# Kernel optimization log

Hardware: AMD Instinct MI355X
Metric: run time of the kernel (lower is better)

The kernel has to match this reference:

```python
import jax, jax.numpy as jnp
import numpy as np

BUCKET_SIZE = 64
N_HASHES = 8
SELF_ATTN_MASK_VAL = -10000.0


def look_one_back(x):
    # concat each chunk with the previous chunk along the within-chunk axis (axis=2)
    prev = jnp.concatenate([x[:, -1:], x[:, :-1]], axis=1)
    return jnp.concatenate([x, prev], axis=2)


def setup_inputs() -> dict:
    key = jax.random.key(0)
    b, s, d = 4, 4096, 64
    n_buckets = s // BUCKET_SIZE  # 64
    kq, kk, kv, kr = jax.random.split(key, 4)
    return {
        "q": jax.random.normal(kq, (b, s, d), jnp.float32),
        "k": jax.random.normal(kk, (b, s, d), jnp.float32),
        "v": jax.random.normal(kv, (b, s, d), jnp.float32),
        "rotations": jax.random.normal(kr, (d, N_HASHES, n_buckets // 2), jnp.float32),
    }


def reference(q, k, v, rotations):
    b, s, d = q.shape
    n_buckets = s // BUCKET_SIZE
    n_chunks = N_HASHES * n_buckets

    # ---- hash_vectors: random-rotation LSH bucketing on q ----
    rot = jnp.einsum('bsd,dhn->bhsn', q, rotations)           # [b, nh, s, nb/2]
    rot = jnp.concatenate([rot, -rot], axis=-1)               # [b, nh, s, nb]
    buckets = jnp.argmax(rot, axis=-1)                        # [b, nh, s]
    offsets = (jnp.arange(N_HASHES) * n_buckets)[None, :, None]
    buckets = (buckets + offsets).reshape(b, N_HASHES * s)    # [b, nh*s]

    # ---- sort tokens by (bucket, position) ----
    ticker = jnp.broadcast_to(jnp.arange(N_HASHES * s), (b, N_HASHES * s))
    buckets_and_t = s * buckets + (ticker % s)
    sticker = jnp.argsort(buckets_and_t, axis=-1)             # sort permutation
    sbuckets_and_t = jnp.take_along_axis(buckets_and_t, sticker, axis=-1)
    undo_sort = jnp.argsort(sticker, axis=-1)
    st = sticker % s                                          # original positions

    gather_seq = lambda x, idx: jnp.take_along_axis(x, idx[..., None], axis=1)
    sq = gather_seq(q, st)
    sk = gather_seq(k, st)
    sv = gather_seq(v, st)

    bq_t = st.reshape(b, n_chunks, -1)                        # [b, n, s_c]
    bq = sq.reshape(b, n_chunks, -1, d)
    bk = sk.reshape(b, n_chunks, -1, d)
    bv = sv.reshape(b, n_chunks, -1, d)

    bk = bk / jnp.linalg.norm(bk, axis=-1, keepdims=True)
    bk = look_one_back(bk)                                    # [b, n, 2*s_c, d]
    bv = look_one_back(bv)
    bkv_t = look_one_back(bq_t)                               # [b, n, 2*s_c]

    dots = jnp.einsum('bnsd,bnzd->bnsz', bq, bk) * (d ** -0.5)
    masked_value = -jnp.finfo(dots.dtype).max

    # self-attention mask (soft, matches torch SELF_ATTN_MASK_VAL)
    self_mask = bq_t[:, :, :, None] == bkv_t[:, :, None, :]
    dots = jnp.where(self_mask, SELF_ATTN_MASK_VAL, dots)

    # do not attend across buckets
    bq_buckets = (sbuckets_and_t // s).reshape(b, n_chunks, -1)
    bkv_buckets = look_one_back(bq_buckets)
    bucket_mask = bq_buckets[:, :, :, None] != bkv_buckets[:, :, None, :]
    dots = jnp.where(bucket_mask, masked_value, dots)

    # duplicate-attention correction
    locs1 = undo_sort // BUCKET_SIZE
    locs2 = (locs1 + 1) % n_chunks
    locs1 = buckets * n_chunks + locs1
    locs2 = buckets * n_chunks + locs2
    locs = jnp.concatenate([locs1.reshape(b, N_HASHES, s),
                            locs2.reshape(b, N_HASHES, s)], axis=1)
    locs = jnp.transpose(locs, (0, 2, 1))                     # [b, s, 2*nh]
    slocs = jnp.take_along_axis(locs, st[..., None], axis=1)  # [b, nh*s, 2*nh]
    b_locs = slocs.reshape(b, n_chunks, -1, 2 * N_HASHES)
    bq_locs = jnp.concatenate([b_locs[..., :N_HASHES], b_locs[..., :N_HASHES]], axis=-1)
    bkv_locs = look_one_back(b_locs)                          # [b, n, 2*s_c, 2*nh]
    dup_counts = jnp.sum(bq_locs[:, :, :, None, :] == bkv_locs[:, :, None, :, :], axis=-1)
    dots = dots - jnp.log(dup_counts.astype(dots.dtype) + 1e-9)

    # softmax (stable) and attention output
    dots_lse = jax.nn.logsumexp(dots, axis=-1, keepdims=True)
    probs_chunk = jnp.exp(dots - dots_lse)
    bo = jnp.einsum('bnsz,bnzd->bnsd', probs_chunk, bv)

    # unsort and combine across hash rounds
    so = bo.reshape(b, -1, d)
    o = jnp.take_along_axis(so, undo_sort[..., None], axis=1).reshape(b, N_HASHES, s, d)
    slogits = dots_lse.reshape(b, -1)
    logits = jnp.take_along_axis(slogits, undo_sort, axis=1).reshape(b, N_HASHES, s, 1)
    probs = jnp.exp(logits - jax.nn.logsumexp(logits, axis=1, keepdims=True))
    out = jnp.sum(o * probs, axis=1)                          # [b, s, d]
    return out
```

## Files before the change

kernel.cpp:

```cpp
#include <hip/hip_runtime.h>
#include <hip/hip_bf16.h>
#include <math.h>

constexpr int B   = 4;
constexpr int S   = 4096;
constexpr int D   = 64;
constexpr int NH  = 8;
constexpr int NB  = 64;
constexpr int NBT = 512;
constexpr int NI  = NH * S;
constexpr int NCH = 512;
constexpr int CHB = 256;

typedef __attribute__((ext_vector_type(8))) _Float16 f16x8;
typedef __attribute__((ext_vector_type(2))) __fp16 fp16x2;
typedef __attribute__((ext_vector_type(4))) float f32x4;
typedef __attribute__((ext_vector_type(2))) unsigned short u16x2;

__device__ __forceinline__ unsigned short f16b(float x) {
    _Float16 h = (_Float16)x;
    return __builtin_bit_cast(unsigned short, h);
}
__device__ __forceinline__ u16x2 nm2(int a, int b) {
    u16x2 x = __builtin_bit_cast(u16x2, a ^ b);
    u16x2 one = {1, 1};
    return __builtin_elementwise_min(x, one);
}
__device__ __forceinline__ unsigned pk16(float a, float b) {
    fp16x2 hp = __builtin_amdgcn_cvt_pkrtz(a, b);
    return __builtin_bit_cast(unsigned, hp);
}
template <int CTRL>
__device__ __forceinline__ float dppf(float x) {
    return __builtin_bit_cast(float,
        __builtin_amdgcn_update_dpp(__builtin_bit_cast(int, x), __builtin_bit_cast(int, x),
                                    CTRL, 0xF, 0xF, false));
}

__global__ void k_prep(const float* __restrict__ q, const float* __restrict__ k,
                       const float* __restrict__ v, unsigned short* __restrict__ q16,
                       unsigned short* __restrict__ kn16, unsigned short* __restrict__ v16) {
    int row  = blockIdx.x * 4 + (threadIdx.x >> 6);
    int lane = threadIdx.x & 63;
    size_t idx = (size_t)row * 64 + lane;
    float kv = k[idx];
    float ss = kv * kv;
#pragma unroll
    for (int m = 1; m < 64; m <<= 1) ss += __shfl_xor(ss, m, 64);
    kn16[idx] = f16b(kv / sqrtf(ss));
    q16[idx]  = f16b(q[idx] * 0.125f);
    v16[idx]  = f16b(v[idx]);
}

__global__ __launch_bounds__(256)
void k_hash(const float* __restrict__ q, const float* __restrict__ rot,
            int* __restrict__ buckets, int* __restrict__ counts) {
    int blk = blockIdx.x;
    int tko = blk & 31, h = (blk >> 5) & 7, b = blk >> 8;
    __shared__ __align__(16) float rs[64 * 36];
    __shared__ int hist[64];
    if (threadIdx.x < 64) hist[threadIdx.x] = 0;
    for (int i = threadIdx.x; i < 2048; i += 256) {
        int nn = i & 31, d = i >> 5;
        rs[d * 36 + nn] = rot[(d * 8 + h) * 32 + nn];
    }
    __syncthreads();
    int tid = threadIdx.x;
    int ng = tid & 7, tg = tid >> 3;
    int t0 = tko * 128 + tg * 4;
    const float* qp = q + ((size_t)b * S + t0) * 64;
    float acc[4][4] = {};
    #pragma unroll 4
    for (int d4 = 0; d4 < 16; ++d4) {
        f32x4 r4[4];
        #pragma unroll
        for (int dd = 0; dd < 4; ++dd)
            r4[dd] = *(const f32x4*)(rs + (4 * d4 + dd) * 36 + 4 * ng);
        #pragma unroll
        for (int i = 0; i < 4; ++i) {
            f32x4 q4 = *(const f32x4*)(qp + i * 64 + d4 * 4);
            #pragma unroll
            for (int dd = 0; dd < 4; ++dd)
                #pragma unroll
                for (int c = 0; c < 4; ++c)
                    acc[i][c] += q4[dd] * r4[dd][c];
        }
    }
    #pragma unroll
    for (int i = 0; i < 4; ++i) {
        float vp = -3.402823466e38f, vn = -3.402823466e38f;
        int ip = 0, in_ = 0;
        #pragma unroll
        for (int c = 0; c < 4; ++c) {
            float a = acc[i][c]; int idx = 4 * ng + c;
            if (a > vp)  { vp = a;  ip = idx; }
            if (-a > vn) { vn = -a; in_ = idx; }
        }
        #pragma unroll
        for (int off = 1; off < 8; off <<= 1) {
            float ov = __shfl_xor(vp, off); int oi = __shfl_xor(ip, off);
            if (ov > vp || (ov == vp && oi < ip)) { vp = ov; ip = oi; }
            ov = __shfl_xor(vn, off); oi = __shfl_xor(in_, off);
            if (ov > vn || (ov == vn && oi < in_)) { vn = ov; in_ = oi; }
        }
        if (ng == 0) {
            int bi = (vn > vp) ? (in_ + 32) : ip;
            buckets[b * NI + h * 4096 + t0 + i] = bi + h * NB;
            atomicAdd(&hist[bi], 1);
        }
    }
    __syncthreads();
    int cglob = h * 32 + tko;
    int* cw = counts + ((size_t)b * CHB + cglob) * NBT;
    for (int j = tid; j < NBT; j += 256) {
        int local = j - h * 64;
        cw[j] = (local >= 0 && local < 64) ? hist[local] : 0;
    }
}

__global__ void k_scan1(int* __restrict__ counts, int* __restrict__ tot) {
    int bkt = blockIdx.x & 511, b = blockIdx.x >> 9;
    int lane = threadIdx.x;
    size_t i0 = ((size_t)b * CHB + 4 * lane) * NBT + bkt;
    int v0 = counts[i0], v1 = counts[i0 + NBT], v2 = counts[i0 + 2 * NBT], v3 = counts[i0 + 3 * NBT];
    int s = v0 + v1 + v2 + v3;
    int incl = s;
    #pragma unroll
    for (int off = 1; off < 64; off <<= 1) {
        int t = __shfl_up(incl, off);
        if (lane >= off) incl += t;
    }
    int excl = incl - s;
    counts[i0]           = excl;
    counts[i0 + NBT]     = excl + v0;
    counts[i0 + 2 * NBT] = excl + v0 + v1;
    counts[i0 + 3 * NBT] = excl + v0 + v1 + v2;
    if (lane == 63) tot[b * NBT + bkt] = incl;
}

__global__ void k_scatter(const int* __restrict__ buckets, const int* __restrict__ counts,
                          const int* __restrict__ tot, int* __restrict__ spos,
                          int* __restrict__ undo) {
    int b = blockIdx.x >> 8, c = blockIdx.x & 255;
    __shared__ int bk_s[128];
    __shared__ int sbase[NBT];
    __shared__ int wsum[2];
    int tid = threadIdx.x;
    int4 tv = *(const int4*)(tot + b * NBT + tid * 4);
    int part = tv.x + tv.y + tv.z + tv.w;
    int incl = part;
    int lane = tid & 63, w = tid >> 6;
    #pragma unroll
    for (int off = 1; off < 64; off <<= 1) {
        int t = __shfl_up(incl, off);
        if (lane >= off) incl += t;
    }
    if (lane == 63) wsum[w] = incl;
    int i_flat = c * 128 + tid;
    int bkt = buckets[b * NI + i_flat];
    bk_s[tid] = bkt;
    __syncthreads();
    if (w == 1) incl += wsum[0];
    int excl = incl - part;
    sbase[4 * tid]     = excl;
    sbase[4 * tid + 1] = excl + tv.x;
    sbase[4 * tid + 2] = excl + tv.x + tv.y;
    sbase[4 * tid + 3] = excl + tv.x + tv.y + tv.z;
    __syncthreads();
    int rank = 0;
    for (int j = 0; j < 128; ++j) {
        int vv = bk_s[j];
        rank += (j < tid && vv == bkt);
    }
    int pos = sbase[bkt] + counts[((size_t)b * CHB + c) * NBT + bkt] + rank;
    spos[b * NI + pos] = (i_flat & 4095) | (bkt << 12);
    undo[b * NI + i_flat] = pos;
}

__global__ void k_locP(const int* __restrict__ buckets, const int* __restrict__ undo,
                       int4* __restrict__ loc1P) {
    int idx = blockIdx.x * 256 + threadIdx.x;
    int b = idx >> 12, t = idx & 4095;
    int v1[8];
    #pragma unroll
    for (int h = 0; h < 8; ++h) {
        int i = b * NI + (h << 12) + t;
        int lo = (buckets[i] & 63) << 9;
        int ch = undo[i] >> 6;
        v1[h] = lo | ch;
    }
    loc1P[idx] = make_int4(v1[0] | (v1[1] << 16), v1[2] | (v1[3] << 16),
                           v1[4] | (v1[5] << 16), v1[6] | (v1[7] << 16));
}

__device__ __forceinline__ int bump_loc(int k1) {
    return (k1 & 0x7E007E00) | ((k1 + 0x00010001) & 0x01FF01FF);
}

__global__ __launch_bounds__(256, 2)
void k_attn(const unsigned short* __restrict__ q16, const unsigned short* __restrict__ kn16,
            const unsigned short* __restrict__ v16, const int* __restrict__ spos,
            const int4* __restrict__ loc1P, unsigned short* __restrict__ soh,
            float* __restrict__ slog) {
    int n = blockIdx.x & 511, b = blockIdx.x >> 9;
    __shared__ __align__(16) char buf[31488];
    unsigned short* qs = (unsigned short*)buf;
    unsigned short* ks = (unsigned short*)(buf + 9216);
    unsigned short* ph = (unsigned short*)buf;
    unsigned short* vh = (unsigned short*)(buf + 9216);
    int* klocs1 = (int*)(buf + 27648);
    int* qlocs  = (int*)(buf + 29696);
    int* mq     = (int*)(buf + 30720);
    int* mk     = (int*)(buf + 30976);

    int tid = threadIdx.x;
    int bni = b * NI;
    const unsigned short* q16b = q16 + ((size_t)b << 12) * 64;
    const unsigned short* kn16b = kn16 + ((size_t)b << 12) * 64;
    const unsigned short* v16b = v16 + ((size_t)b << 12) * 64;

    if (tid < 64) mq[tid] = spos[bni + n * 64 + tid];
    else if (tid < 192) {
        int z = tid - 64;
        int nn = (z < 64) ? n : ((n + 511) & 511);
        mk[z] = spos[bni + nn * 64 + (z & 63)];
    }
    __syncthreads();

    #pragma unroll
    for (int it = 0; it < 2; ++it) {
        int i = it * 256 + tid;
        int row = i >> 3, c8 = i & 7;
        int t = mq[row] & 4095;
        uint4 val = *(const uint4*)(q16b + (size_t)t * 64 + c8 * 8);
        *(uint4*)(qs + row * 72 + c8 * 8) = val;
    }
    #pragma unroll
    for (int it = 0; it < 4; ++it) {
        int i = it * 256 + tid;
        int row = i >> 3, c8 = i & 7;
        int t = mk[row] & 4095;
        uint4 val = *(const uint4*)(kn16b + (size_t)t * 64 + c8 * 8);
        *(uint4*)(ks + row * 72 + c8 * 8) = val;
    }
    if (tid < 128) {
        int t = mk[tid] & 4095;
        *(int4*)(klocs1 + tid * 4) = loc1P[((size_t)b << 12) | t];
    } else if (tid < 192) {
        int r = tid - 128;
        int tq = mq[r] & 4095;
        *(int4*)(qlocs + r * 4) = loc1P[((size_t)b << 12) | tq];
    }
    __syncthreads();

    int li = tid & 15, hi4 = (tid >> 4) & 3, w = tid >> 6;

    f32x4 sacc[8];
    {
        f16x8 a0 = *(f16x8*)(qs + (16 * w + li) * 72 + 8 * hi4);
        f16x8 a1 = *(f16x8*)(qs + (16 * w + li) * 72 + 32 + 8 * hi4);
        #pragma unroll
        for (int zt = 0; zt < 8; ++zt) {
            f16x8 b0 = *(f16x8*)(ks + (16 * zt + li) * 72 + 8 * hi4);
            f16x8 b1 = *(f16x8*)(ks + (16 * zt + li) * 72 + 32 + 8 * hi4);
            f32x4 c = {0.f, 0.f, 0.f, 0.f};
            c = __builtin_amdgcn_mfma_f32_16x16x32_f16(a0, b0, c, 0, 0, 0);
            c = __builtin_amdgcn_mfma_f32_16x16x32_f16(a1, b1, c, 0, 0, 0);
            sacc[zt] = c;
        }
    }

    int tqr[4], bqr[4];
    int4 lq[4];
    #pragma unroll
    for (int j = 0; j < 4; ++j) {
        int R = 16 * w + 4 * hi4 + j;
        int m = mq[R];
        tqr[j] = m & 4095; bqr[j] = m >> 12;
        lq[j] = *(const int4*)(qlocs + R * 4);
    }
    #pragma unroll
    for (int zt = 0; zt < 8; ++zt) {
        int z = 16 * zt + li;
        int mz = mk[z]; int tk = mz & 4095, bk = mz >> 12;
        int4 k1 = *(const int4*)(klocs1 + z * 4);
        int4 k2;
        k2.x = bump_loc(k1.x); k2.y = bump_loc(k1.y);
        k2.z = bump_loc(k1.z); k2.w = bump_loc(k1.w);
        #pragma unroll
        for (int j = 0; j < 4; ++j) {
            float s = sacc[zt][j];
            if (tqr[j] == tk) s = -10000.0f;
            if (bqr[j] != bk) s = -3.402823466e38f;
            u16x2 acc = nm2(lq[j].x, k1.x);
            acc = acc + nm2(lq[j].y, k1.y);
            acc = acc + nm2(lq[j].z, k1.z);
            acc = acc + nm2(lq[j].w, k1.w);
            acc = acc + nm2(lq[j].x, k2.x);
            acc = acc + nm2(lq[j].y, k2.y);
            acc = acc + nm2(lq[j].z, k2.z);
            acc = acc + nm2(lq[j].w, k2.w);
            unsigned ua = __builtin_bit_cast(unsigned, acc);
            int dup = 16 - (int)((ua & 0xffffu) + (ua >> 16));
            s -= __logf(fmaxf((float)dup, 1.0f));
            sacc[zt][j] = s;
        }
    }

    float inv[4];
    #pragma unroll
    for (int j = 0; j < 4; ++j) {
        float m = sacc[0][j];
        #pragma unroll
        for (int zt = 1; zt < 8; ++zt) m = fmaxf(m, sacc[zt][j]);
        m = fmaxf(m, dppf<0x121>(m));
        m = fmaxf(m, dppf<0x122>(m));
        m = fmaxf(m, dppf<0x124>(m));
        m = fmaxf(m, dppf<0x128>(m));
        float sum = 0.f;
        #pragma unroll
        for (int zt = 0; zt < 8; ++zt) {
            float e = __expf(sacc[zt][j] - m);
            sacc[zt][j] = e; sum += e;
        }
        sum += dppf<0x121>(sum);
        sum += dppf<0x122>(sum);
        sum += dppf<0x124>(sum);
        sum += dppf<0x128>(sum);
        float lse = m + __logf(sum);
        inv[j] = 1.0f / sum;
        if (li == 0) slog[bni + n * 64 + 16 * w + 4 * hi4 + j] = lse;
    }
    __syncthreads();

    #pragma unroll
    for (int it = 0; it < 8; ++it) {
        int i = it * 256 + tid;
        int zp = i & 63;
        int dp = i >> 6;
        int t0 = mk[2 * zp] & 4095, t1 = mk[2 * zp + 1] & 4095;
        unsigned a = *(const unsigned*)(v16b + (size_t)t0 * 64 + 2 * dp);
        unsigned c = *(const unsigned*)(v16b + (size_t)t1 * 64 + 2 * dp);
        *(unsigned*)(vh + (2 * dp) * 136 + 2 * zp)     = __builtin_amdgcn_perm(c, a, 0x05040100u);
        *(unsigned*)(vh + (2 * dp + 1) * 136 + 2 * zp) = __builtin_amdgcn_perm(c, a, 0x07060302u);
    }
    f32x4 oacc[4] = {{0,0,0,0},{0,0,0,0},{0,0,0,0},{0,0,0,0}};
    #pragma unroll
    for (int half = 0; half < 2; ++half) {
        #pragma unroll
        for (int zt4 = 0; zt4 < 4; ++zt4) {
            int zt = half * 4 + zt4;
            #pragma unroll
            for (int j = 0; j < 4; ++j) {
                float p  = sacc[zt][j] * inv[j];
                float po = dppf<0xB1>(p);
                if ((li & 1) == 0) {
                    int R  = 16 * w + 4 * hi4 + j;
                    int zl = 16 * zt4 + li;
                    *(unsigned*)(ph + R * 72 + zl) = pk16(p, po);
                }
            }
        }
        __syncthreads();
        #pragma unroll
        for (int step = 0; step < 2; ++step) {
            f16x8 pa = *(f16x8*)(ph + (16 * w + li) * 72 + 32 * step + 8 * hi4);
            #pragma unroll
            for (int nt = 0; nt < 4; ++nt) {
                f16x8 vb = *(f16x8*)(vh + (16 * nt + li) * 136 + 64 * half + 32 * step + 8 * hi4);
                oacc[nt] = __builtin_amdgcn_mfma_f32_16x16x32_f16(pa, vb, oacc[nt], 0, 0, 0);
            }
        }
        __syncthreads();
    }

    size_t ob = ((size_t)bni + n * 64) * 64;
    #pragma unroll
    for (int nt = 0; nt < 4; ++nt)
        #pragma unroll
        for (int j = 0; j < 4; ++j) {
            float o  = oacc[nt][j];
            float oo = dppf<0xB1>(o);
            if ((li & 1) == 0) {
                *(unsigned*)(soh + ob + (size_t)(16 * w + 4 * hi4 + j) * 64 + 16 * nt + li) =
                    pk16(o, oo);
            }
        }
}

__global__ void k_comb(const int* __restrict__ undo, const float* __restrict__ slog,
                       const unsigned short* __restrict__ soh, float* __restrict__ out) {
    int flatT = blockIdx.x * 4 + (threadIdx.x >> 6);
    int lane  = threadIdx.x & 63;
    int b = flatT >> 12, t = flatT & (S - 1);
    int ph[NH]; float lg[NH];
    float m = -3.402823466e38f;
#pragma unroll
    for (int h = 0; h < NH; ++h) {
        ph[h] = undo[b * NI + (h << 12) + t];
        lg[h] = slog[b * NI + ph[h]];
        m = fmaxf(m, lg[h]);
    }
    float sum = 0.f;
#pragma unroll
    for (int h = 0; h < NH; ++h) sum += __expf(lg[h] - m);
    float lse2 = m + __logf(sum);
    float o = 0.f;
#pragma unroll
    for (int h = 0; h < NH; ++h) {
        float wgt = __expf(lg[h] - lse2);
        _Float16 hv = *(const _Float16*)(soh + ((size_t)b * NI + ph[h]) * D + lane);
        o += wgt * (float)hv;
    }
    out[(size_t)flatT * D + lane] = o;
}

extern "C" void kernel_launch(void* const* d_in, const int* in_sizes, int n_in,
                              void* d_out, int out_size, void* d_ws, size_t ws_size,
                              hipStream_t stream) {
    const float* q   = (const float*)d_in[0];
    const float* k   = (const float*)d_in[1];
    const float* v   = (const float*)d_in[2];
    const float* rot = (const float*)d_in[3];
    float* out = (float*)d_out;

    char* ws = (char*)d_ws;
    size_t off = 0;
    auto alloc = [&](size_t bytes) -> void* {
        void* p = ws + off;
        off += (bytes + 255) & ~(size_t)255;
        return p;
    };
    unsigned short* q16  = (unsigned short*)alloc((size_t)B * S * D * 2);
    unsigned short* kn16 = (unsigned short*)alloc((size_t)B * S * D * 2);
    unsigned short* v16  = (unsigned short*)alloc((size_t)B * S * D * 2);
    unsigned short* soh  = (unsigned short*)alloc((size_t)B * NI * D * 2);
    float* slog    = (float*)alloc((size_t)B * NI * 4);
    int*   buckets = (int*)alloc((size_t)B * NI * 4);
    int*   counts  = (int*)alloc((size_t)B * CHB * NBT * 4);
    int*   tot     = (int*)alloc((size_t)B * NBT * 4);
    int*   spos    = (int*)alloc((size_t)B * NI * 4);
    int*   undo    = (int*)alloc((size_t)B * NI * 4);
    int4*  loc1P   = (int4*)alloc((size_t)B * S * 16);

    k_prep<<<B * S / 4, 256, 0, stream>>>(q, k, v, q16, kn16, v16);
    k_hash<<<1024, 256, 0, stream>>>(q, rot, buckets, counts);
    k_scan1<<<B * NBT, 64, 0, stream>>>(counts, tot);
    k_scatter<<<B * CHB, 128, 0, stream>>>(buckets, counts, tot, spos, undo);
    k_locP<<<B * S / 256, 256, 0, stream>>>(buckets, undo, loc1P);
    k_attn<<<B * NCH, 256, 0, stream>>>(q16, kn16, v16, spos, loc1P, soh, slog);
    k_comb<<<B * S / 4, 256, 0, stream>>>(undo, slog, soh, out);
}
```

Before: 106.4 us.

## Fuse prep, scan and loc kernels into hash/scatter and switch softmax to base-2

```diff
diff --git a/kernel.cpp b/kernel.cpp
--- a/kernel.cpp
+++ b/kernel.cpp
@@ -17,9 +17,14 @@
 typedef __attribute__((ext_vector_type(4))) float f32x4;
 typedef __attribute__((ext_vector_type(2))) unsigned short u16x2;
 
+constexpr float LOG2E = 1.44269504088896341f;
+
 __device__ __forceinline__ unsigned short f16b(float x) {
     _Float16 h = (_Float16)x;
     return __builtin_bit_cast(unsigned short, h);
+}
+__device__ __forceinline__ unsigned pk_rne(float a, float b) {
+    return (unsigned)f16b(a) | ((unsigned)f16b(b) << 16);
 }
 __device__ __forceinline__ u16x2 nm2(int a, int b) {
     u16x2 x = __builtin_bit_cast(u16x2, a ^ b);
@@ -37,35 +42,23 @@
                                     CTRL, 0xF, 0xF, false));
 }
 
-__global__ void k_prep(const float* __restrict__ q, const float* __restrict__ k,
-                       const float* __restrict__ v, unsigned short* __restrict__ q16,
-                       unsigned short* __restrict__ kn16, unsigned short* __restrict__ v16) {
-    int row  = blockIdx.x * 4 + (threadIdx.x >> 6);
-    int lane = threadIdx.x & 63;
-    size_t idx = (size_t)row * 64 + lane;
-    float kv = k[idx];
-    float ss = kv * kv;
-#pragma unroll
-    for (int m = 1; m < 64; m <<= 1) ss += __shfl_xor(ss, m, 64);
-    kn16[idx] = f16b(kv / sqrtf(ss));
-    q16[idx]  = f16b(q[idx] * 0.125f);
-    v16[idx]  = f16b(v[idx]);
-}
-
 __global__ __launch_bounds__(256)
-void k_hash(const float* __restrict__ q, const float* __restrict__ rot,
-            int* __restrict__ buckets, int* __restrict__ counts) {
+void k_hash(const float* __restrict__ q, const float* __restrict__ k,
+            const float* __restrict__ v, const float* __restrict__ rot,
+            int* __restrict__ buckets, int* __restrict__ counts, int* __restrict__ tot,
+            unsigned short* __restrict__ q16, unsigned short* __restrict__ kn16,
+            unsigned short* __restrict__ v16) {
     int blk = blockIdx.x;
     int tko = blk & 31, h = (blk >> 5) & 7, b = blk >> 8;
     __shared__ __align__(16) float rs[64 * 36];
     __shared__ int hist[64];
-    if (threadIdx.x < 64) hist[threadIdx.x] = 0;
-    for (int i = threadIdx.x; i < 2048; i += 256) {
+    int tid = threadIdx.x;
+    if (tid < 64) hist[tid] = 0;
+    for (int i = tid; i < 2048; i += 256) {
         int nn = i & 31, d = i >> 5;
         rs[d * 36 + nn] = rot[(d * 8 + h) * 32 + nn];
     }
     __syncthreads();
-    int tid = threadIdx.x;
     int ng = tid & 7, tg = tid >> 3;
     int t0 = tko * 128 + tg * 4;
     const float* qp = q + ((size_t)b * S + t0) * 64;
@@ -110,55 +103,95 @@
         }
     }
     __syncthreads();
-    int cglob = h * 32 + tko;
-    int* cw = counts + ((size_t)b * CHB + cglob) * NBT;
-    for (int j = tid; j < NBT; j += 256) {
-        int local = j - h * 64;
-        cw[j] = (local >= 0 && local < 64) ? hist[local] : 0;
-    }
-}
-
-__global__ void k_scan1(int* __restrict__ counts, int* __restrict__ tot) {
-    int bkt = blockIdx.x & 511, b = blockIdx.x >> 9;
-    int lane = threadIdx.x;
-    size_t i0 = ((size_t)b * CHB + 4 * lane) * NBT + bkt;
-    int v0 = counts[i0], v1 = counts[i0 + NBT], v2 = counts[i0 + 2 * NBT], v3 = counts[i0 + 3 * NBT];
-    int s = v0 + v1 + v2 + v3;
-    int incl = s;
-    #pragma unroll
-    for (int off = 1; off < 64; off <<= 1) {
-        int t = __shfl_up(incl, off);
-        if (lane >= off) incl += t;
-    }
-    int excl = incl - s;
-    counts[i0]           = excl;
-    counts[i0 + NBT]     = excl + v0;
-    counts[i0 + 2 * NBT] = excl + v0 + v1;
-    counts[i0 + 3 * NBT] = excl + v0 + v1 + v2;
-    if (lane == 63) tot[b * NBT + bkt] = incl;
+    if (tid < 64) {
+        int cnt = hist[tid];
+        counts[((size_t)b * NBT + h * 64 + tid) * 32 + tko] = cnt;
+        atomicAdd(&tot[b * NBT + h * 64 + tid], cnt);
+    }
+
+    if (h == 0) {
+        int r  = tko * 128 + (tid >> 1);
+        int hf = tid & 1;
+        size_t base = ((size_t)b * S + r) * 64 + hf * 32;
+        f32x4 rv[8];
+        float ss = 0.f;
+        #pragma unroll
+        for (int j = 0; j < 8; ++j) {
+            rv[j] = *(const f32x4*)(k + base + 4 * j);
+            ss += rv[j][0]*rv[j][0] + rv[j][1]*rv[j][1] + rv[j][2]*rv[j][2] + rv[j][3]*rv[j][3];
+        }
+        ss += __shfl_xor(ss, 1);
+        float sc = rsqrtf(ss);
+        unsigned ow[16];
+        #pragma unroll
+        for (int i = 0; i < 16; ++i) {
+            float a  = rv[i >> 1][(i & 1) * 2] * sc;
+            float bb = rv[i >> 1][(i & 1) * 2 + 1] * sc;
+            ow[i] = pk_rne(a, bb);
+        }
+        *(uint4*)(kn16 + base)      = make_uint4(ow[0], ow[1], ow[2], ow[3]);
+        *(uint4*)(kn16 + base + 8)  = make_uint4(ow[4], ow[5], ow[6], ow[7]);
+        *(uint4*)(kn16 + base + 16) = make_uint4(ow[8], ow[9], ow[10], ow[11]);
+        *(uint4*)(kn16 + base + 24) = make_uint4(ow[12], ow[13], ow[14], ow[15]);
+        const float qsc = 0.125f * LOG2E;
+        #pragma unroll
+        for (int j = 0; j < 8; ++j) rv[j] = *(const f32x4*)(q + base + 4 * j);
+        #pragma unroll
+        for (int i = 0; i < 16; ++i)
+            ow[i] = pk_rne(rv[i >> 1][(i & 1) * 2] * qsc, rv[i >> 1][(i & 1) * 2 + 1] * qsc);
+        *(uint4*)(q16 + base)      = make_uint4(ow[0], ow[1], ow[2], ow[3]);
+        *(uint4*)(q16 + base + 8)  = make_uint4(ow[4], ow[5], ow[6], ow[7]);
+        *(uint4*)(q16 + base + 16) = make_uint4(ow[8], ow[9], ow[10], ow[11]);
+        *(uint4*)(q16 + base + 24) = make_uint4(ow[12], ow[13], ow[14], ow[15]);
+        #pragma unroll
+        for (int j = 0; j < 8; ++j) rv[j] = *(const f32x4*)(v + base + 4 * j);
+        #pragma unroll
+        for (int i = 0; i < 16; ++i)
+            ow[i] = pk_rne(rv[i >> 1][(i & 1) * 2], rv[i >> 1][(i & 1) * 2 + 1]);
+        *(uint4*)(v16 + base)      = make_uint4(ow[0], ow[1], ow[2], ow[3]);
+        *(uint4*)(v16 + base + 8)  = make_uint4(ow[4], ow[5], ow[6], ow[7]);
+        *(uint4*)(v16 + base + 16) = make_uint4(ow[8], ow[9], ow[10], ow[11]);
+        *(uint4*)(v16 + base + 24) = make_uint4(ow[12], ow[13], ow[14], ow[15]);
+    }
 }
 
 __global__ void k_scatter(const int* __restrict__ buckets, const int* __restrict__ counts,
                           const int* __restrict__ tot, int* __restrict__ spos,
-                          int* __restrict__ undo) {
+                          int* __restrict__ undo, unsigned short* __restrict__ locU) {
     int b = blockIdx.x >> 8, c = blockIdx.x & 255;
+    int h = c >> 5, tko = c & 31;
     __shared__ int bk_s[128];
     __shared__ int sbase[NBT];
+    __shared__ int pfx[64];
     __shared__ int wsum[2];
     int tid = threadIdx.x;
+    int lane = tid & 63, w = tid >> 6;
     int4 tv = *(const int4*)(tot + b * NBT + tid * 4);
     int part = tv.x + tv.y + tv.z + tv.w;
     int incl = part;
-    int lane = tid & 63, w = tid >> 6;
     #pragma unroll
     for (int off = 1; off < 64; off <<= 1) {
-        int t = __shfl_up(incl, off);
-        if (lane >= off) incl += t;
+        int t_ = __shfl_up(incl, off);
+        if (lane >= off) incl += t_;
     }
     if (lane == 63) wsum[w] = incl;
+    int bl = tid >> 1, hf = tid & 1;
+    const int* crow = counts + ((size_t)b * NBT + h * 64 + bl) * 32 + hf * 16;
+    int ps = 0;
+    #pragma unroll
+    for (int jj = 0; jj < 4; ++jj) {
+        int4 cv = *(const int4*)(crow + jj * 4);
+        int bi = hf * 16 + jj * 4;
+        ps += (bi + 0 < tko) ? cv.x : 0;
+        ps += (bi + 1 < tko) ? cv.y : 0;
+        ps += (bi + 2 < tko) ? cv.z : 0;
+        ps += (bi + 3 < tko) ? cv.w : 0;
+    }
+    ps += __shfl_xor(ps, 1);
     int i_flat = c * 128 + tid;
     int bkt = buckets[b * NI + i_flat];
     bk_s[tid] = bkt;
+    if (hf == 0) pfx[bl] = ps;
     __syncthreads();
     if (w == 1) incl += wsum[0];
     int excl = incl - part;
@@ -172,25 +205,12 @@
         int vv = bk_s[j];
         rank += (j < tid && vv == bkt);
     }
-    int pos = sbase[bkt] + counts[((size_t)b * CHB + c) * NBT + bkt] + rank;
+    int pos = sbase[bkt] + pfx[bkt - h * 64] + rank;
     spos[b * NI + pos] = (i_flat & 4095) | (bkt << 12);
     undo[b * NI + i_flat] = pos;
-}
-
-__global__ void k_locP(const int* __restrict__ buckets, const int* __restrict__ undo,
-                       int4* __restrict__ loc1P) {
-    int idx = blockIdx.x * 256 + threadIdx.x;
-    int b = idx >> 12, t = idx & 4095;
-    int v1[8];
-    #pragma unroll
-    for (int h = 0; h < 8; ++h) {
-        int i = b * NI + (h << 12) + t;
-        int lo = (buckets[i] & 63) << 9;
-        int ch = undo[i] >> 6;
-        v1[h] = lo | ch;
-    }
-    loc1P[idx] = make_int4(v1[0] | (v1[1] << 16), v1[2] | (v1[3] << 16),
-                           v1[4] | (v1[5] << 16), v1[6] | (v1[7] << 16));
+    int t = i_flat & 4095;
+    locU[(((size_t)b << 12) | t) * 8 + h] =
+        (unsigned short)(((bkt & 63) << 9) | (pos >> 6));
 }
 
 __device__ __forceinline__ int bump_loc(int k1) {
@@ -290,7 +310,7 @@
         #pragma unroll
         for (int j = 0; j < 4; ++j) {
             float s = sacc[zt][j];
-            if (tqr[j] == tk) s = -10000.0f;
+            if (tqr[j] == tk) s = -14426.950408f;
             if (bqr[j] != bk) s = -3.402823466e38f;
             u16x2 acc = nm2(lq[j].x, k1.x);
             acc = acc + nm2(lq[j].y, k1.y);
@@ -302,7 +322,7 @@
             acc = acc + nm2(lq[j].w, k2.w);
             unsigned ua = __builtin_bit_cast(unsigned, acc);
             int dup = 16 - (int)((ua & 0xffffu) + (ua >> 16));
-            s -= __logf(fmaxf((float)dup, 1.0f));
+            s -= log2f(fmaxf((float)dup, 1.0f));
             sacc[zt][j] = s;
         }
     }
@@ -320,15 +340,15 @@
         float sum = 0.f;
         #pragma unroll
         for (int zt = 0; zt < 8; ++zt) {
-            float e = __expf(sacc[zt][j] - m);
+            float e = exp2f(sacc[zt][j] - m);
             sacc[zt][j] = e; sum += e;
         }
         sum += dppf<0x121>(sum);
         sum += dppf<0x122>(sum);
         sum += dppf<0x124>(sum);
         sum += dppf<0x128>(sum);
-        float lse = m + __logf(sum);
-        inv[j] = 1.0f / sum;
+        float lse = m + log2f(sum);
+        inv[j] = __builtin_amdgcn_rcpf(sum);
         if (li == 0) slog[bni + n * 64 + 16 * w + 4 * hi4 + j] = lse;
     }
     __syncthreads();
@@ -403,12 +423,12 @@
     }
     float sum = 0.f;
 #pragma unroll
-    for (int h = 0; h < NH; ++h) sum += __expf(lg[h] - m);
-    float lse2 = m + __logf(sum);
+    for (int h = 0; h < NH; ++h) sum += exp2f(lg[h] - m);
+    float lse2 = m + log2f(sum);
     float o = 0.f;
 #pragma unroll
     for (int h = 0; h < NH; ++h) {
-        float wgt = __expf(lg[h] - lse2);
+        float wgt = exp2f(lg[h] - lse2);
         _Float16 hv = *(const _Float16*)(soh + ((size_t)b * NI + ph[h]) * D + lane);
         o += wgt * (float)hv;
     }
@@ -437,17 +457,15 @@
     unsigned short* soh  = (unsigned short*)alloc((size_t)B * NI * D * 2);
     float* slog    = (float*)alloc((size_t)B * NI * 4);
     int*   buckets = (int*)alloc((size_t)B * NI * 4);
-    int*   counts  = (int*)alloc((size_t)B * CHB * NBT * 4);
+    int*   counts  = (int*)alloc((size_t)B * NBT * 32 * 4);
     int*   tot     = (int*)alloc((size_t)B * NBT * 4);
     int*   spos    = (int*)alloc((size_t)B * NI * 4);
     int*   undo    = (int*)alloc((size_t)B * NI * 4);
-    int4*  loc1P   = (int4*)alloc((size_t)B * S * 16);
-
-    k_prep<<<B * S / 4, 256, 0, stream>>>(q, k, v, q16, kn16, v16);
-    k_hash<<<1024, 256, 0, stream>>>(q, rot, buckets, counts);
-    k_scan1<<<B * NBT, 64, 0, stream>>>(counts, tot);
-    k_scatter<<<B * CHB, 128, 0, stream>>>(buckets, counts, tot, spos, undo);
-    k_locP<<<B * S / 256, 256, 0, stream>>>(buckets, undo, loc1P);
-    k_attn<<<B * NCH, 256, 0, stream>>>(q16, kn16, v16, spos, loc1P, soh, slog);
+    unsigned short* locU = (unsigned short*)alloc((size_t)B * S * NH * 2);
+
+    hipMemsetAsync(tot, 0, (size_t)B * NBT * 4, stream);
+    k_hash<<<1024, 256, 0, stream>>>(q, k, v, rot, buckets, counts, tot, q16, kn16, v16);
+    k_scatter<<<B * CHB, 128, 0, stream>>>(buckets, counts, tot, spos, undo, locU);
+    k_attn<<<B * NCH, 256, 0, stream>>>(q16, kn16, v16, spos, (const int4*)locU, soh, slog);
     k_comb<<<B * S / 4, 256, 0, stream>>>(undo, slog, soh, out);
 }
```

Result: slower. 110.7 us (+4.0%).
